# Kernel optimization log

Hardware: AMD Instinct MI355X
Metric: run time of the kernel (lower is better)

Reference implementation:

```python
import jax, jax.numpy as jnp
import numpy as np

B, S, D, H, L, OUT = 4, 1024, 1024, 16, 6, 512
HD = D // H
EPS = 1e-5


def _positional_encoding(seq, dim):
    pos = np.arange(seq, dtype=np.float32)[:, None]          # [S,1]
    i = np.arange(0, dim, 2, dtype=np.float32)[None, :]       # even indices
    div = np.power(10000.0, 2.0 * i / dim)                    # repo's (nonstandard) exponent
    pe = np.zeros((seq, dim), dtype=np.float32)
    pe[:, 0::2] = np.sin(pos / div)
    pe[:, 1::2] = np.cos(pos / div)
    return jnp.asarray(pe)[None]                               # [1,S,D]


def _causal_mask(seq):
    r = jnp.arange(seq)
    m = jnp.where(r[None, :] > r[:, None], jnp.float32(-jnp.inf), jnp.float32(0.0))
    return m[None, None]                                       # [1,1,S,S]


def setup_inputs() -> dict:
    key = jax.random.key(0)
    ks = jax.random.split(key, 10)
    sc = 0.02
    inp = {
        'x':      jax.random.normal(ks[0], (B, S, D), jnp.float32),
        'pe':     _positional_encoding(S, D),
        'mask':   _causal_mask(S),
        'ln1_g':  jnp.ones((L, D), jnp.float32),
        'ln1_b':  jnp.zeros((L, D), jnp.float32),
        'wq':     jax.random.normal(ks[1], (L, D, D), jnp.float32) * sc,
        'wk':     jax.random.normal(ks[2], (L, D, D), jnp.float32) * sc,
        'wv':     jax.random.normal(ks[3], (L, D, D), jnp.float32) * sc,
        'wo':     jax.random.normal(ks[4], (L, D, D), jnp.float32) * sc,
        'ln2_g':  jnp.ones((L, D), jnp.float32),
        'ln2_b':  jnp.zeros((L, D), jnp.float32),
        'wf':     jax.random.normal(ks[5], (L, D, D), jnp.float32) * sc,
        'lnf_g':  jnp.ones((D,), jnp.float32),
        'lnf_b':  jnp.zeros((D,), jnp.float32),
        'w_out':  jax.random.normal(ks[6], (OUT, D), jnp.float32) * sc,
    }
    return inp


def _layer_norm(x, g, b):
    mu = jnp.mean(x, axis=-1, keepdims=True)
    var = jnp.mean(jnp.square(x - mu), axis=-1, keepdims=True)
    return (x - mu) * jax.lax.rsqrt(var + EPS) * g + b


def _split_heads(x):
    b, s, d = x.shape
    return x.reshape(b, s, H, HD).transpose(0, 2, 1, 3)  # [B,H,S,HD]


def reference(x, pe, mask, ln1_g, ln1_b, wq, wk, wv, wo, ln2_g, ln2_b, wf, lnf_g, lnf_b, w_out):
    h = x + pe
    scale = 1.0 / jnp.sqrt(jnp.float32(HD))
    for l in range(wq.shape[0]):
        h_ = _layer_norm(h, ln1_g[l], ln1_b[l])
        q = _split_heads(jnp.einsum('bsd,ed->bse', h_, wq[l]))
        k = _split_heads(jnp.einsum('bsd,ed->bse', h_, wk[l]))
        v = _split_heads(jnp.einsum('bsd,ed->bse', h_, wv[l]))
        scores = jnp.einsum('bhqd,bhkd->bhqk', q, k) * scale + mask  # [B,H,S,S]
        probs = jax.nn.softmax(scores, axis=-1)
        attn = jnp.einsum('bhqk,bhkd->bhqd', probs, v)
        attn = attn.transpose(0, 2, 1, 3).reshape(h.shape)            # combine heads
        h = h + jnp.einsum('bsd,ed->bse', attn, wo[l])
        h_ = _layer_norm(h, ln2_g[l], ln2_b[l])
        h = h + jnp.einsum('bsd,ed->bse', h_, wf[l])                  # FFN = plain linear (no activation, as in source)
    h = _layer_norm(h, lnf_g, lnf_b)
    return jnp.einsum('bsd,od->bso', h, w_out)
```

## Files before the change

### kernel.cpp

```cpp
#include <hip/hip_runtime.h>
#include <hip/hip_bf16.h>
#include <stdint.h>

#define BATCH 4
#define SEQ   1024
#define DIM   1024
#define NH    16
#define HDIM  64
#define NLAYER 6
#define NOUT  512
#define NTOK  (BATCH*SEQ)
#define LOG2E 1.44269504088896f
#define NEG_BIG (-1e30f)
#define VTS   72

using bf16 = __hip_bfloat16;
typedef __attribute__((ext_vector_type(4))) float f32x4;
typedef __attribute__((ext_vector_type(8))) short bf16x8;

typedef __attribute__((address_space(1))) void as1_void;
typedef __attribute__((address_space(3))) void as3_void;

__device__ __forceinline__ float bf2f(short u) {
  union { unsigned int i; float f; } c;
  c.i = ((unsigned int)(unsigned short)u) << 16;
  return c.f;
}

__device__ __forceinline__ short f2bs(float f) {
  bf16 h = __float2bfloat16(f);
  return *(short*)&h;
}

__device__ __forceinline__ float exp_clamped(float x) {
  return exp2f(fmaxf(x, -100.f) * LOG2E);
}

__device__ __forceinline__ float loadf(const void* p, size_t i, bool f32) {
  return f32 ? ((const float*)p)[i] : __bfloat162float(((const bf16*)p)[i]);
}

__device__ __forceinline__ void g2l16(const void* g, void* l) {
  __builtin_amdgcn_global_load_lds((const as1_void*)g, (as3_void*)l, 16, 0, 0);
}

__global__ void sniff(const unsigned int* __restrict__ w, int* __restrict__ flag) {
  const int lane = threadIdx.x;
  const unsigned int word = w[lane];
  const int e2 = (word >> 7) & 0xFF;
  const bool bf16ish = (e2 >= 0x60) && (e2 <= 0x8F);
  const unsigned long long m = __ballot(bf16ish);
  if (lane == 0) *flag = (__popcll(m) >= 48) ? 0 : 1;
}

__global__ __launch_bounds__(256) void convert_all(
    const float* __restrict__ s0, const float* __restrict__ s1,
    const float* __restrict__ s2, const float* __restrict__ s3,
    const float* __restrict__ s4, const float* __restrict__ s5,
    bf16* __restrict__ d0, bf16* __restrict__ d1, bf16* __restrict__ d2,
    bf16* __restrict__ d3, bf16* __restrict__ d4, bf16* __restrict__ d5,
    const int* __restrict__ flag) {
  if (*flag == 0) return;
  int b = blockIdx.x;
  const float* s; bf16* d;
  if      (b <  768) { s = s0; d = d0; }
  else if (b < 1536) { s = s1; d = d1; b -= 768; }
  else if (b < 2304) { s = s2; d = d2; b -= 1536; }
  else if (b < 3072) { s = s3; d = d3; b -= 2304; }
  else if (b < 3840) { s = s4; d = d4; b -= 3072; }
  else               { s = s5; d = d5; b -= 3840; }
  const size_t e0 = ((size_t)b * 1024 + threadIdx.x) * 8;
  f32x4 a[4], c[4];
#pragma unroll
  for (int i = 0; i < 4; ++i) {
    a[i] = *(const f32x4*)(s + e0 + i * 2048);
    c[i] = *(const f32x4*)(s + e0 + i * 2048 + 4);
  }
#pragma unroll
  for (int i = 0; i < 4; ++i) {
    bf16x8 o;
    o[0] = f2bs(a[i][0]); o[1] = f2bs(a[i][1]); o[2] = f2bs(a[i][2]); o[3] = f2bs(a[i][3]);
    o[4] = f2bs(c[i][0]); o[5] = f2bs(c[i][1]); o[6] = f2bs(c[i][2]); o[7] = f2bs(c[i][3]);
    *(bf16x8*)(d + e0 + i * 2048) = o;
  }
}

template<int EPI>
__device__ __forceinline__ void gemm_body(const bf16* __restrict__ A,
                                          const bf16* __restrict__ W,
                                          void* __restrict__ C,
                                          const int* __restrict__ flag,
                                          int N, int m0, int n0) {
  __shared__ __align__(16) bf16 lA[128 * 32];
  __shared__ __align__(16) bf16 lB[128 * 32];
  const int tid  = threadIdx.x;
  const int wave = tid >> 6;
  const int lane = tid & 63;
  const int quad = lane >> 4;
  const int l16  = lane & 15;
  const int wm = (wave >> 1) * 64;
  const int wn = (wave & 1) * 64;
  const int K = DIM;

  const int r0 = tid >> 2;
  const int c0 = (tid & 3) * 8;
  const int r1 = (tid + 256) >> 2;

  bool f32out = false;
  if (EPI == 2) f32out = (*flag != 0);

  f32x4 acc[4][4];
#pragma unroll
  for (int i = 0; i < 4; ++i)
#pragma unroll
    for (int j = 0; j < 4; ++j) acc[i][j] = (f32x4){0.f, 0.f, 0.f, 0.f};

  for (int k0 = 0; k0 < K; k0 += 32) {
    __syncthreads();
    g2l16(A + (size_t)(m0 + r0) * K + k0 + c0, lA + 512 * wave);
    g2l16(A + (size_t)(m0 + r1) * K + k0 + c0, lA + 2048 + 512 * wave);
    g2l16(W + (size_t)(n0 + r0) * K + k0 + c0, lB + 512 * wave);
    g2l16(W + (size_t)(n0 + r1) * K + k0 + c0, lB + 2048 + 512 * wave);
    __builtin_amdgcn_s_waitcnt(0);
    __syncthreads();

    bf16x8 af[4], bfr[4];
#pragma unroll
    for (int i = 0; i < 4; ++i) {
      af[i]  = *(const bf16x8*)(lA + (wm + i * 16 + l16) * 32 + quad * 8);
      bfr[i] = *(const bf16x8*)(lB + (wn + i * 16 + l16) * 32 + quad * 8);
    }
#pragma unroll
    for (int i = 0; i < 4; ++i)
#pragma unroll
      for (int j = 0; j < 4; ++j)
        acc[i][j] = __builtin_amdgcn_mfma_f32_16x16x32_bf16(af[i], bfr[j], acc[i][j], 0, 0, 0);
  }

#pragma unroll
  for (int i = 0; i < 4; ++i) {
    const int rowb = m0 + wm + i * 16 + quad * 4;
#pragma unroll
    for (int j = 0; j < 4; ++j) {
      const int col = n0 + wn + j * 16 + l16;
#pragma unroll
      for (int r = 0; r < 4; ++r) {
        const size_t idx = (size_t)(rowb + r) * N + col;
        const float v = acc[i][j][r];
        if (EPI == 0) ((bf16*)C)[idx] = __float2bfloat16(v);
        else { if (f32out) ((float*)C)[idx] = v; else ((bf16*)C)[idx] = __float2bfloat16(v); }
      }
    }
  }
}

__global__ __launch_bounds__(256) void gemm_out(const bf16* __restrict__ A,
                                                const bf16* __restrict__ Wc,
                                                const bf16* __restrict__ Wo,
                                                void* __restrict__ C,
                                                const int* __restrict__ flag) {
  const int obid = blockIdx.x;
  const int wid = (obid & 7) * 16 + (obid >> 3);
  const int m0 = (wid & 31) * 128;
  const int n0 = (wid >> 5) * 128;
  const bf16* W = (*flag != 0) ? Wc : Wo;
  gemm_body<2>(A, W, C, flag, NOUT, m0, n0);
}

__global__ __launch_bounds__(256) void gemm_qkv(const bf16* __restrict__ A,
                                                const bf16* __restrict__ cq,
                                                const bf16* __restrict__ ck,
                                                const bf16* __restrict__ cvv,
                                                const bf16* __restrict__ oq,
                                                const bf16* __restrict__ ok,
                                                const bf16* __restrict__ ov,
                                                bf16* __restrict__ q,
                                                bf16* __restrict__ k,
                                                bf16* __restrict__ v,
                                                const int* __restrict__ flag) {
  const int obid = blockIdx.x;
  const int wid = (obid & 7) * 96 + (obid >> 3);
  const int m0   = (wid & 31) * 128;
  const int rest = wid >> 5;
  const int sel  = rest >> 3;
  const int n0   = (rest & 7) * 128;
  const bool f32 = (*flag != 0);
  const bf16* W = (sel == 0) ? (f32 ? cq : oq)
                 : (sel == 1) ? (f32 ? ck : ok)
                              : (f32 ? cvv : ov);
  bf16* C = (sel == 0) ? q : (sel == 1 ? k : v);
  gemm_body<0>(A, W, C, nullptr, DIM, m0, n0);
}

__device__ __forceinline__ void gemm64_body(const bf16* __restrict__ A,
                                            const bf16* __restrict__ W,
                                            float* __restrict__ C,
                                            int N, int m0, int n0) {
  __shared__ __align__(16) bf16 lA[64 * 32];
  __shared__ __align__(16) bf16 lB[128 * 32];
  const int tid  = threadIdx.x;
  const int wave = tid >> 6;
  const int lane = tid & 63;
  const int quad = lane >> 4;
  const int l16  = lane & 15;
  const int wm = (wave >> 1) * 32;
  const int wn = (wave & 1) * 64;
  const int K = DIM;

  const int r0 = tid >> 2;
  const int c0 = (tid & 3) * 8;
  const int r1 = (tid + 256) >> 2;

  f32x4 acc[2][4];
#pragma unroll
  for (int i = 0; i < 2; ++i)
#pragma unroll
    for (int j = 0; j < 4; ++j) acc[i][j] = (f32x4){0.f, 0.f, 0.f, 0.f};

  for (int k0 = 0; k0 < K; k0 += 32) {
    __syncthreads();
    g2l16(A + (size_t)(m0 + r0) * K + k0 + c0, lA + 512 * wave);
    g2l16(W + (size_t)(n0 + r0) * K + k0 + c0, lB + 512 * wave);
    g2l16(W + (size_t)(n0 + r1) * K + k0 + c0, lB + 2048 + 512 * wave);
    __builtin_amdgcn_s_waitcnt(0);
    __syncthreads();

    bf16x8 af[2], bfr[4];
#pragma unroll
    for (int i = 0; i < 2; ++i)
      af[i]  = *(const bf16x8*)(lA + (wm + i * 16 + l16) * 32 + quad * 8);
#pragma unroll
    for (int j = 0; j < 4; ++j)
      bfr[j] = *(const bf16x8*)(lB + (wn + j * 16 + l16) * 32 + quad * 8);
#pragma unroll
    for (int i = 0; i < 2; ++i)
#pragma unroll
      for (int j = 0; j < 4; ++j)
        acc[i][j] = __builtin_amdgcn_mfma_f32_16x16x32_bf16(af[i], bfr[j], acc[i][j], 0, 0, 0);
  }

#pragma unroll
  for (int i = 0; i < 2; ++i) {
    const int rowb = m0 + wm + i * 16 + quad * 4;
#pragma unroll
    for (int j = 0; j < 4; ++j) {
      const int col = n0 + wn + j * 16 + l16;
#pragma unroll
      for (int r = 0; r < 4; ++r)
        C[(size_t)(rowb + r) * N + col] += acc[i][j][r];
    }
  }
}

__global__ __launch_bounds__(256) void gemm_add(const bf16* __restrict__ A,
                                                const bf16* __restrict__ Wc,
                                                const bf16* __restrict__ Wo,
                                                const int* __restrict__ flag,
                                                float* __restrict__ C) {
  const int obid = blockIdx.x;
  const int wid = (obid & 7) * 64 + (obid >> 3);
  const int m0 = (wid & 63) * 64;
  const int n0 = (wid >> 6) * 128;
  const bf16* W = (*flag != 0) ? Wc : Wo;
  gemm64_body(A, W, C, DIM, m0, n0);
}

__global__ __launch_bounds__(256) void add_pe(const void* __restrict__ x,
                                              const void* __restrict__ pe,
                                              float* __restrict__ h,
                                              const int* __restrict__ flag) {
  const bool f32 = (*flag != 0);
  const size_t i = (size_t)blockIdx.x * 256 + threadIdx.x;
  h[i] = loadf(x, i, f32) + loadf(pe, i & (SEQ * DIM - 1), f32);
}

__global__ __launch_bounds__(256) void layernorm(const float* __restrict__ x,
                                                 const void* __restrict__ g,
                                                 const void* __restrict__ b,
                                                 int loff,
                                                 bf16* __restrict__ y,
                                                 const int* __restrict__ flag) {
  const bool f32 = (*flag != 0);
  const int row = blockIdx.x;
  const int tid = threadIdx.x;
  const int wave = tid >> 6;
  const float* xr = x + (size_t)row * DIM;
  __shared__ float red[8];

  float v[4];
  float s = 0.f;
#pragma unroll
  for (int i = 0; i < 4; ++i) { v[i] = xr[tid + 256 * i]; s += v[i]; }
#pragma unroll
  for (int off = 32; off >= 1; off >>= 1) s += __shfl_xor(s, off);
  if ((tid & 63) == 0) red[wave] = s;
  __syncthreads();
  const float mu = (red[0] + red[1] + red[2] + red[3]) * (1.f / DIM);

  float vs = 0.f;
#pragma unroll
  for (int i = 0; i < 4; ++i) { const float d = v[i] - mu; vs += d * d; }
#pragma unroll
  for (int off = 32; off >= 1; off >>= 1) vs += __shfl_xor(vs, off);
  if ((tid & 63) == 0) red[4 + wave] = vs;
  __syncthreads();
  const float var = (red[4] + red[5] + red[6] + red[7]) * (1.f / DIM);
  const float rs = rsqrtf(var + 1e-5f);

#pragma unroll
  for (int i = 0; i < 4; ++i) {
    const int d = tid + 256 * i;
    const float gv = loadf(g, (size_t)loff + d, f32);
    const float bv = loadf(b, (size_t)loff + d, f32);
    y[(size_t)row * DIM + d] = __float2bfloat16((v[i] - mu) * rs * gv + bv);
  }
}

__global__ __launch_bounds__(256, 2) void attn_flash(const bf16* __restrict__ q,
                                                     const bf16* __restrict__ k,
                                                     const bf16* __restrict__ v,
                                                     bf16* __restrict__ o) {
  __shared__ __align__(16) short lK[64 * 64];
  __shared__ __align__(16) short lVT[64 * VTS];
  __shared__ __align__(16) short lP[4 * 16 * VTS];

  const int obid = blockIdx.x;
  const int wid = (obid & 7) * 128 + (obid >> 3);
  const int bh = wid >> 4;
  const int qt = 15 - (wid & 15);
  const int hh = bh & (NH - 1);
  const int bb = bh >> 4;
  const int q0 = qt * 64;

  const int tid = threadIdx.x;
  const int wave = tid >> 6;
  const int lane = tid & 63;
  const int quad = lane >> 4;
  const int l16 = lane & 15;

  const size_t base = (size_t)bb * SEQ * DIM + hh * HDIM;
  const int qlo = q0 + wave * 16;

  bf16x8 qf[2];
  {
    const bf16* qr = q + base + (size_t)(qlo + l16) * DIM;
#pragma unroll
    for (int kc = 0; kc < 2; ++kc) {
      bf16x8 t = *(const bf16x8*)(qr + kc * 32 + quad * 8);
      bf16x8 sq;
#pragma unroll
      for (int e = 0; e < 8; ++e) sq[e] = f2bs(bf2f(t[e]) * 0.125f);
      qf[kc] = sq;
    }
  }

  float l_acc[4] = {0.f, 0.f, 0.f, 0.f};
  f32x4 oacc[4];
#pragma unroll
  for (int nb = 0; nb < 4; ++nb) oacc[nb] = (f32x4){0.f, 0.f, 0.f, 0.f};

  short* lPw = lP + wave * 16 * VTS;
  const int nt = qt + 1;

  for (int t = 0; t < nt; ++t) {
    const int kbase = t * 64;
    __syncthreads();

    {
      const int r8 = lane >> 3;
      const int cc = (lane & 7) ^ r8;
#pragma unroll
      for (int c = 0; c < 2; ++c) {
        const int row = wave * 16 + c * 8 + r8;
        g2l16(k + base + (size_t)(kbase + row) * DIM + cc * 8,
              lK + (wave * 16 + c * 8) * 64);
      }
    }

    bf16x8 vch[2];
#pragma unroll
    for (int c2 = 0; c2 < 2; ++c2) {
      const int cid = tid + c2 * 256;
      const int kk = cid >> 3;
      const int d0 = (cid & 7) * 8;
      vch[c2] = *(const bf16x8*)(v + base + (size_t)(kbase + kk) * DIM + d0);
    }
#pragma unroll
    for (int c2 = 0; c2 < 2; ++c2) {
      const int cid = tid + c2 * 256;
      const int kk = cid >> 3;
      const int d0 = (cid & 7) * 8;
#pragma unroll
      for (int e = 0; e < 8; ++e) {
        const int d = d0 + e;
        const int kks = kk ^ (((d >> 3) & 7) << 3);
        lVT[d * VTS + kks] = vch[c2][e];
      }
    }
    __builtin_amdgcn_s_waitcnt(0);
    __syncthreads();

    f32x4 s[4];
#pragma unroll
    for (int nb = 0; nb < 4; ++nb) {
      f32x4 acc = (f32x4){0.f, 0.f, 0.f, 0.f};
      const int n = nb * 16 + l16;
#pragma unroll
      for (int kc = 0; kc < 2; ++kc) {
        const int cidx = (kc * 4 + quad) ^ (n & 7);
        bf16x8 kf = *(const bf16x8*)(lK + n * 64 + cidx * 8);
        acc = __builtin_amdgcn_mfma_f32_16x16x32_bf16(qf[kc], kf, acc, 0, 0, 0);
      }
      s[nb] = acc;
    }

    if (kbase + 63 > qlo) {
#pragma unroll
      for (int nb = 0; nb < 4; ++nb) {
        const int j = kbase + nb * 16 + l16;
#pragma unroll
        for (int r = 0; r < 4; ++r)
          if (j > qlo + quad * 4 + r) s[nb][r] = NEG_BIG;
      }
    }

#pragma unroll
    for (int nb = 0; nb < 4; ++nb) {
#pragma unroll
      for (int r = 0; r < 4; ++r) {
        const float p = exp_clamped(s[nb][r]);
        l_acc[r] += p;
        lPw[(quad * 4 + r) * VTS + nb * 16 + l16] = f2bs(p);
      }
    }

    __builtin_amdgcn_s_waitcnt(0);
    bf16x8 pf[2];
#pragma unroll
    for (int kc = 0; kc < 2; ++kc)
      pf[kc] = *(const bf16x8*)(lPw + l16 * VTS + kc * 32 + quad * 8);

#pragma unroll
    for (int nb = 0; nb < 4; ++nb) {
      const int n = nb * 16 + l16;
      const int swz = ((n >> 3) & 7) << 3;
#pragma unroll
      for (int kc = 0; kc < 2; ++kc) {
        const int kchunk = (kc * 32 + quad * 8) ^ swz;
        bf16x8 vf = *(const bf16x8*)(lVT + n * VTS + kchunk);
        oacc[nb] = __builtin_amdgcn_mfma_f32_16x16x32_bf16(pf[kc], vf, oacc[nb], 0, 0, 0);
      }
    }
  }

  float linv[4];
#pragma unroll
  for (int r = 0; r < 4; ++r) {
    float ts = l_acc[r];
#pragma unroll
    for (int off = 8; off >= 1; off >>= 1) ts += __shfl_xor(ts, off);
    linv[r] = 1.f / ts;
  }
#pragma unroll
  for (int nb = 0; nb < 4; ++nb)
#pragma unroll
    for (int r = 0; r < 4; ++r) {
      const int qrow = q0 + wave * 16 + quad * 4 + r;
      o[base + (size_t)qrow * DIM + nb * 16 + l16] =
          __float2bfloat16(oacc[nb][r] * linv[r]);
    }
}

extern "C" void kernel_launch(void* const* d_in, const int* in_sizes, int n_in,
                              void* d_out, int out_size, void* d_ws, size_t ws_size,
                              hipStream_t stream) {
  const void* x    = d_in[0];
  const void* pe   = d_in[1];
  const void* ln1g = d_in[3];
  const void* ln1b = d_in[4];
  const void* wq   = d_in[5];
  const void* wk   = d_in[6];
  const void* wv   = d_in[7];
  const void* wo   = d_in[8];
  const void* ln2g = d_in[9];
  const void* ln2b = d_in[10];
  const void* wf   = d_in[11];
  const void* lnfg = d_in[12];
  const void* lnfb = d_in[13];
  const void* wout = d_in[14];

  const size_t MB = 1u << 20;
  char* ws = (char*)d_ws;
  int*  flag = (int*)ws;
  bf16* wqc  = (bf16*)(ws + 1 * MB);
  bf16* wkc  = (bf16*)(ws + 13 * MB);
  bf16* wvc  = (bf16*)(ws + 25 * MB);
  bf16* woc  = (bf16*)(ws + 37 * MB);
  bf16* wfc  = (bf16*)(ws + 49 * MB);
  bf16* woutc= (bf16*)(ws + 61 * MB);
  float* h   = (float*)(ws + 62 * MB);
  bf16* hn   = (bf16*)(ws + 78 * MB);
  bf16* qb   = (bf16*)(ws + 86 * MB);
  bf16* kb   = (bf16*)(ws + 94 * MB);
  bf16* vb   = (bf16*)(ws + 102 * MB);
  bf16* ab   = hn;

  sniff<<<1, 64, 0, stream>>>((const unsigned int*)wq, flag);

  convert_all<<<3904, 256, 0, stream>>>(
      (const float*)wq, (const float*)wk, (const float*)wv,
      (const float*)wo, (const float*)wf, (const float*)wout,
      wqc, wkc, wvc, woc, wfc, woutc, flag);

  add_pe<<<NTOK * DIM / 256, 256, 0, stream>>>(x, pe, h, flag);

  for (int l = 0; l < NLAYER; ++l) {
    const size_t woff = (size_t)l << 20;
    const int poff = l * DIM;
    layernorm<<<NTOK, 256, 0, stream>>>(h, ln1g, ln1b, poff, hn, flag);
    gemm_qkv<<<dim3(768), 256, 0, stream>>>(
        hn, wqc + woff, wkc + woff, wvc + woff,
        (const bf16*)wq + woff, (const bf16*)wk + woff, (const bf16*)wv + woff,
        qb, kb, vb, flag);
    attn_flash<<<dim3(BATCH * NH * (SEQ / 64)), 256, 0, stream>>>(qb, kb, vb, ab);
    gemm_add<<<dim3(512), 256, 0, stream>>>(ab, woc + woff,
                                            (const bf16*)wo + woff, flag, h);
    layernorm<<<NTOK, 256, 0, stream>>>(h, ln2g, ln2b, poff, hn, flag);
    gemm_add<<<dim3(512), 256, 0, stream>>>(hn, wfc + woff,
                                            (const bf16*)wf + woff, flag, h);
  }

  layernorm<<<NTOK, 256, 0, stream>>>(h, lnfg, lnfb, 0, hn, flag);
  gemm_out<<<dim3(128), 256, 0, stream>>>(hn, woutc, (const bf16*)wout,
                                          d_out, flag);
}
```

Before: 1.042 ms.

## Double GEMM K-step to 64 with XOR-swizzled LDS panels and simplify block mapping

Both GEMM bodies now stage a K=64 slice per iteration, as two 32-wide panels, which halves the number of barrier and waitcnt round trips in the K loop. The LDS layout is XOR-swizzled so fragment reads avoid bank conflicts. The XCD-aware block remapping in the GEMM and attention kernels is replaced with a plain 2D grid and a simple linear mapping. The cost is double the LDS per block and a loss of the L2 locality the old XCD swizzle may have provided.

```diff
diff --git a/kernel.cpp b/kernel.cpp
--- a/kernel.cpp
+++ b/kernel.cpp
@@ -85,14 +85,20 @@
   }
 }
 
+__device__ __forceinline__ bf16x8 rd_frag(const short* panel, int row, int quad) {
+  const int g  = row >> 1;
+  const int cc = (((row & 1) << 2) | quad) ^ (g & 7);
+  return *(const bf16x8*)(panel + g * 64 + cc * 8);
+}
+
 template<int EPI>
 __device__ __forceinline__ void gemm_body(const bf16* __restrict__ A,
                                           const bf16* __restrict__ W,
                                           void* __restrict__ C,
                                           const int* __restrict__ flag,
                                           int N, int m0, int n0) {
-  __shared__ __align__(16) bf16 lA[128 * 32];
-  __shared__ __align__(16) bf16 lB[128 * 32];
+  __shared__ __align__(16) short lA[8192];
+  __shared__ __align__(16) short lB[8192];
   const int tid  = threadIdx.x;
   const int wave = tid >> 6;
   const int lane = tid & 63;
@@ -102,9 +108,10 @@
   const int wn = (wave & 1) * 64;
   const int K = DIM;
 
-  const int r0 = tid >> 2;
-  const int c0 = (tid & 3) * 8;
-  const int r1 = (tid + 256) >> 2;
+  const int c3   = (lane & 7) ^ (lane >> 3);
+  const int sq   = (c3 & 3) * 8;
+  const int rsub = ((lane >> 3) << 1) | (c3 >> 2);
+  const int ldsW = wave * 512;
 
   bool f32out = false;
   if (EPI == 2) f32out = (*flag != 0);
@@ -115,26 +122,37 @@
 #pragma unroll
     for (int j = 0; j < 4; ++j) acc[i][j] = (f32x4){0.f, 0.f, 0.f, 0.f};
 
-  for (int k0 = 0; k0 < K; k0 += 32) {
+  for (int k0 = 0; k0 < K; k0 += 64) {
     __syncthreads();
-    g2l16(A + (size_t)(m0 + r0) * K + k0 + c0, lA + 512 * wave);
-    g2l16(A + (size_t)(m0 + r1) * K + k0 + c0, lA + 2048 + 512 * wave);
-    g2l16(W + (size_t)(n0 + r0) * K + k0 + c0, lB + 512 * wave);
-    g2l16(W + (size_t)(n0 + r1) * K + k0 + c0, lB + 2048 + 512 * wave);
+#pragma unroll
+    for (int kc = 0; kc < 2; ++kc)
+#pragma unroll
+      for (int c = 0; c < 2; ++c) {
+        const int row = c * 64 + wave * 16 + rsub;
+        g2l16(A + (size_t)(m0 + row) * K + k0 + kc * 32 + sq,
+              lA + kc * 4096 + c * 2048 + ldsW);
+        g2l16(W + (size_t)(n0 + row) * K + k0 + kc * 32 + sq,
+              lB + kc * 4096 + c * 2048 + ldsW);
+      }
     __builtin_amdgcn_s_waitcnt(0);
     __syncthreads();
 
-    bf16x8 af[4], bfr[4];
-#pragma unroll
-    for (int i = 0; i < 4; ++i) {
-      af[i]  = *(const bf16x8*)(lA + (wm + i * 16 + l16) * 32 + quad * 8);
-      bfr[i] = *(const bf16x8*)(lB + (wn + i * 16 + l16) * 32 + quad * 8);
-    }
-#pragma unroll
-    for (int i = 0; i < 4; ++i)
-#pragma unroll
-      for (int j = 0; j < 4; ++j)
-        acc[i][j] = __builtin_amdgcn_mfma_f32_16x16x32_bf16(af[i], bfr[j], acc[i][j], 0, 0, 0);
+#pragma unroll
+    for (int kc = 0; kc < 2; ++kc) {
+      const short* pA = lA + kc * 4096;
+      const short* pB = lB + kc * 4096;
+      bf16x8 af[4], bfr[4];
+#pragma unroll
+      for (int i = 0; i < 4; ++i) {
+        af[i]  = rd_frag(pA, wm + i * 16 + l16, quad);
+        bfr[i] = rd_frag(pB, wn + i * 16 + l16, quad);
+      }
+#pragma unroll
+      for (int i = 0; i < 4; ++i)
+#pragma unroll
+        for (int j = 0; j < 4; ++j)
+          acc[i][j] = __builtin_amdgcn_mfma_f32_16x16x32_bf16(af[i], bfr[j], acc[i][j], 0, 0, 0);
+    }
   }
 
 #pragma unroll
@@ -159,12 +177,8 @@
                                                 const bf16* __restrict__ Wo,
                                                 void* __restrict__ C,
                                                 const int* __restrict__ flag) {
-  const int obid = blockIdx.x;
-  const int wid = (obid & 7) * 16 + (obid >> 3);
-  const int m0 = (wid & 31) * 128;
-  const int n0 = (wid >> 5) * 128;
   const bf16* W = (*flag != 0) ? Wc : Wo;
-  gemm_body<2>(A, W, C, flag, NOUT, m0, n0);
+  gemm_body<2>(A, W, C, flag, NOUT, blockIdx.y * 128, blockIdx.x * 128);
 }
 
 __global__ __launch_bounds__(256) void gemm_qkv(const bf16* __restrict__ A,
@@ -178,26 +192,23 @@
                                                 bf16* __restrict__ k,
                                                 bf16* __restrict__ v,
                                                 const int* __restrict__ flag) {
-  const int obid = blockIdx.x;
-  const int wid = (obid & 7) * 96 + (obid >> 3);
-  const int m0   = (wid & 31) * 128;
-  const int rest = wid >> 5;
-  const int sel  = rest >> 3;
-  const int n0   = (rest & 7) * 128;
+  const int gx = blockIdx.x;
+  const int sel = gx >> 3;
+  const int n0 = (gx & 7) * 128;
   const bool f32 = (*flag != 0);
   const bf16* W = (sel == 0) ? (f32 ? cq : oq)
                  : (sel == 1) ? (f32 ? ck : ok)
                               : (f32 ? cvv : ov);
   bf16* C = (sel == 0) ? q : (sel == 1 ? k : v);
-  gemm_body<0>(A, W, C, nullptr, DIM, m0, n0);
+  gemm_body<0>(A, W, C, nullptr, DIM, blockIdx.y * 128, n0);
 }
 
 __device__ __forceinline__ void gemm64_body(const bf16* __restrict__ A,
                                             const bf16* __restrict__ W,
                                             float* __restrict__ C,
                                             int N, int m0, int n0) {
-  __shared__ __align__(16) bf16 lA[64 * 32];
-  __shared__ __align__(16) bf16 lB[128 * 32];
+  __shared__ __align__(16) short lA[4096];
+  __shared__ __align__(16) short lB[8192];
   const int tid  = threadIdx.x;
   const int wave = tid >> 6;
   const int lane = tid & 63;
@@ -207,9 +218,10 @@
   const int wn = (wave & 1) * 64;
   const int K = DIM;
 
-  const int r0 = tid >> 2;
-  const int c0 = (tid & 3) * 8;
-  const int r1 = (tid + 256) >> 2;
+  const int c3   = (lane & 7) ^ (lane >> 3);
+  const int sq   = (c3 & 3) * 8;
+  const int rsub = ((lane >> 3) << 1) | (c3 >> 2);
+  const int ldsW = wave * 512;
 
   f32x4 acc[2][4];
 #pragma unroll
@@ -217,26 +229,40 @@
 #pragma unroll
     for (int j = 0; j < 4; ++j) acc[i][j] = (f32x4){0.f, 0.f, 0.f, 0.f};
 
-  for (int k0 = 0; k0 < K; k0 += 32) {
+  for (int k0 = 0; k0 < K; k0 += 64) {
     __syncthreads();
-    g2l16(A + (size_t)(m0 + r0) * K + k0 + c0, lA + 512 * wave);
-    g2l16(W + (size_t)(n0 + r0) * K + k0 + c0, lB + 512 * wave);
-    g2l16(W + (size_t)(n0 + r1) * K + k0 + c0, lB + 2048 + 512 * wave);
+#pragma unroll
+    for (int kc = 0; kc < 2; ++kc) {
+      const int arow = wave * 16 + rsub;
+      g2l16(A + (size_t)(m0 + arow) * K + k0 + kc * 32 + sq,
+            lA + kc * 2048 + ldsW);
+#pragma unroll
+      for (int c = 0; c < 2; ++c) {
+        const int brow = c * 64 + wave * 16 + rsub;
+        g2l16(W + (size_t)(n0 + brow) * K + k0 + kc * 32 + sq,
+              lB + kc * 4096 + c * 2048 + ldsW);
+      }
+    }
     __builtin_amdgcn_s_waitcnt(0);
     __syncthreads();
 
-    bf16x8 af[2], bfr[4];
-#pragma unroll
-    for (int i = 0; i < 2; ++i)
-      af[i]  = *(const bf16x8*)(lA + (wm + i * 16 + l16) * 32 + quad * 8);
-#pragma unroll
-    for (int j = 0; j < 4; ++j)
-      bfr[j] = *(const bf16x8*)(lB + (wn + j * 16 + l16) * 32 + quad * 8);
-#pragma unroll
-    for (int i = 0; i < 2; ++i)
+#pragma unroll
+    for (int kc = 0; kc < 2; ++kc) {
+      const short* pA = lA + kc * 2048;
+      const short* pB = lB + kc * 4096;
+      bf16x8 af[2], bfr[4];
+#pragma unroll
+      for (int i = 0; i < 2; ++i)
+        af[i] = rd_frag(pA, wm + i * 16 + l16, quad);
 #pragma unroll
       for (int j = 0; j < 4; ++j)
-        acc[i][j] = __builtin_amdgcn_mfma_f32_16x16x32_bf16(af[i], bfr[j], acc[i][j], 0, 0, 0);
+        bfr[j] = rd_frag(pB, wn + j * 16 + l16, quad);
+#pragma unroll
+      for (int i = 0; i < 2; ++i)
+#pragma unroll
+        for (int j = 0; j < 4; ++j)
+          acc[i][j] = __builtin_amdgcn_mfma_f32_16x16x32_bf16(af[i], bfr[j], acc[i][j], 0, 0, 0);
+    }
   }
 
 #pragma unroll
@@ -257,12 +283,8 @@
                                                 const bf16* __restrict__ Wo,
                                                 const int* __restrict__ flag,
                                                 float* __restrict__ C) {
-  const int obid = blockIdx.x;
-  const int wid = (obid & 7) * 64 + (obid >> 3);
-  const int m0 = (wid & 63) * 64;
-  const int n0 = (wid >> 6) * 128;
   const bf16* W = (*flag != 0) ? Wc : Wo;
-  gemm64_body(A, W, C, DIM, m0, n0);
+  gemm64_body(A, W, C, DIM, blockIdx.y * 64, blockIdx.x * 128);
 }
 
 __global__ __launch_bounds__(256) void add_pe(const void* __restrict__ x,
@@ -324,10 +346,9 @@
   __shared__ __align__(16) short lVT[64 * VTS];
   __shared__ __align__(16) short lP[4 * 16 * VTS];
 
-  const int obid = blockIdx.x;
-  const int wid = (obid & 7) * 128 + (obid >> 3);
-  const int bh = wid >> 4;
-  const int qt = 15 - (wid & 15);
+  const int idx = blockIdx.x;
+  const int qt = (SEQ / 64 - 1) - (idx >> 6);
+  const int bh = idx & 63;
   const int hh = bh & (NH - 1);
   const int bb = bh >> 4;
   const int q0 = qt * 64;
@@ -518,19 +539,19 @@
     const size_t woff = (size_t)l << 20;
     const int poff = l * DIM;
     layernorm<<<NTOK, 256, 0, stream>>>(h, ln1g, ln1b, poff, hn, flag);
-    gemm_qkv<<<dim3(768), 256, 0, stream>>>(
+    gemm_qkv<<<dim3(24, 32), 256, 0, stream>>>(
         hn, wqc + woff, wkc + woff, wvc + woff,
         (const bf16*)wq + woff, (const bf16*)wk + woff, (const bf16*)wv + woff,
         qb, kb, vb, flag);
     attn_flash<<<dim3(BATCH * NH * (SEQ / 64)), 256, 0, stream>>>(qb, kb, vb, ab);
-    gemm_add<<<dim3(512), 256, 0, stream>>>(ab, woc + woff,
-                                            (const bf16*)wo + woff, flag, h);
+    gemm_add<<<dim3(8, 64), 256, 0, stream>>>(ab, woc + woff,
+                                              (const bf16*)wo + woff, flag, h);
     layernorm<<<NTOK, 256, 0, stream>>>(h, ln2g, ln2b, poff, hn, flag);
-    gemm_add<<<dim3(512), 256, 0, stream>>>(hn, wfc + woff,
-                                            (const bf16*)wf + woff, flag, h);
+    gemm_add<<<dim3(8, 64), 256, 0, stream>>>(hn, wfc + woff,
+                                              (const bf16*)wf + woff, flag, h);
   }
 
   layernorm<<<NTOK, 256, 0, stream>>>(h, lnfg, lnfb, 0, hn, flag);
-  gemm_out<<<dim3(128), 256, 0, stream>>>(hn, woutc, (const bf16*)wout,
-                                          d_out, flag);
-}
+  gemm_out<<<dim3(4, 32), 256, 0, stream>>>(hn, woutc, (const bf16*)wout,
+                                            d_out, flag);
+}
```

Measured after the change: 914.0 us. 12.3% less time.
